# Performance work log

Measured on AMD Instinct MI355X. Metric: run time of the kernel, lower is better.

Reference implementation:

```python
import jax, jax.numpy as jnp
import numpy as np

B, T, N, D, H, L = 8, 200, 512, 4, 64, 32


def setup_inputs() -> dict:
    key = jax.random.key(0)
    ks = jax.random.split(key, 7)
    s = 1.0 / np.sqrt(H)  # torch GRU/Linear default init scale
    x = jax.random.normal(ks[0], (B, T, N, D), dtype=jnp.float32)
    W_ih = jax.random.uniform(ks[1], (3 * H, D), minval=-s, maxval=s, dtype=jnp.float32)
    W_hh = jax.random.uniform(ks[2], (3 * H, H), minval=-s, maxval=s, dtype=jnp.float32)
    b_ih = jax.random.uniform(ks[3], (3 * H,), minval=-s, maxval=s, dtype=jnp.float32)
    b_hh = jax.random.uniform(ks[4], (3 * H,), minval=-s, maxval=s, dtype=jnp.float32)
    W_enc = jax.random.uniform(ks[5], (L, H), minval=-s, maxval=s, dtype=jnp.float32)
    b_enc = jax.random.uniform(ks[6], (L,), minval=-s, maxval=s, dtype=jnp.float32)
    return {"trajectories": x, "W_ih": W_ih, "W_hh": W_hh, "b_ih": b_ih,
            "b_hh": b_hh, "W_enc": W_enc, "b_enc": b_enc}


def _gru_last_hidden(x, W_ih, W_hh, b_ih, b_hh):
    # x: [M, T, D] -> last hidden [M, H]; PyTorch GRU gate order (r, z, n)
    gx = jnp.einsum('mtd,gd->mtg', x, W_ih) + b_ih  # [M, T, 3H], input gates precomputed

    def step(h, gxt):
        gh = h @ W_hh.T + b_hh                      # [M, 3H]
        rz = jax.nn.sigmoid(gxt[:, :2 * H] + gh[:, :2 * H])
        r, z = rz[:, :H], rz[:, H:]
        n = jnp.tanh(gxt[:, 2 * H:] + r * gh[:, 2 * H:])
        h = (1.0 - z) * n + z * h
        return h, None

    h0 = jnp.zeros((x.shape[0], H), dtype=x.dtype)
    hT, _ = jax.lax.scan(step, h0, jnp.swapaxes(gx, 0, 1))  # scan over T
    return hT


def reference(trajectories, W_ih, W_hh, b_ih, b_hh, W_enc, b_enc):
    b, t, n, d = trajectories.shape
    # permute(1,0,2) per clip == move object axis before time, flatten all trajectories
    x = jnp.transpose(trajectories, (0, 2, 1, 3)).reshape(b * n, t, d)  # [M, T, D]
    hT = _gru_last_hidden(x, W_ih, W_hh, b_ih, b_hh)                    # [M, H]
    out = hT @ W_enc.T + b_enc                                          # [M, L]
    return out.reshape(b, n, L)  # list of [N, L] per clip, stacked
```

## Files before the change

kernel.cpp:

```cpp
#include <hip/hip_runtime.h>

#define TT 200
#define NN 512
#define DD 4
#define HH 64
#define LL 32
#define SB 16
#define BPB (NN / SB)
#define KP 72
#define LOG2E 1.44269504088896340736f

typedef short bf16x8 __attribute__((ext_vector_type(8)));
typedef float f32x4 __attribute__((ext_vector_type(4)));

union U8 { unsigned short s[8]; unsigned u[4]; bf16x8 v; };

__device__ __forceinline__ void split2(float x, unsigned short& hi, unsigned short& lo) {
    unsigned u = __float_as_uint(x);
    hi = (unsigned short)(u >> 16);
    float lf = x - __uint_as_float(u & 0xffff0000u);
    lo = (unsigned short)(__float_as_uint(lf) >> 16);
}

__global__ __launch_bounds__(256, 1)
void gru_traj_kernel(const float* __restrict__ xg,
                     const float* __restrict__ W_ih,
                     const float* __restrict__ W_hh,
                     const float* __restrict__ b_ih,
                     const float* __restrict__ b_hh,
                     const float* __restrict__ W_enc,
                     const float* __restrict__ b_enc,
                     float* __restrict__ out)
{
    __shared__ __align__(16) unsigned short hhi[2][SB][KP];
    __shared__ __align__(16) unsigned short hlo[2][SB][KP];
    __shared__ __align__(16) float hsf[SB][HH + 4];

    const int tid = threadIdx.x;
    const int bid = blockIdx.x;
    const int b   = bid >> 5;
    const int n0  = (bid & (BPB - 1)) * SB;

    const int w  = tid >> 6;
    const int l  = tid & 63;
    const int lr = l & 15;
    const int lg = l >> 4;
    const int u0 = 16 * w + lg * 4;

    const float sc[3] = { LOG2E, LOG2E, 2.0f * LOG2E };

    bf16x8 awh[3][2];
    #pragma unroll
    for (int i = 0; i < 3; ++i) {
        const int g = i * 64 + 16 * w + lr;
        #pragma unroll
        for (int kc = 0; kc < 2; ++kc) {
            const float* p = W_hh + g * HH + kc * 32 + lg * 8;
            U8 uh;
            #pragma unroll
            for (int j = 0; j < 8; ++j) {
                unsigned short hi, lo;
                split2(p[j] * sc[i], hi, lo);
                uh.s[j] = hi; (void)lo;
            }
            awh[i][kc] = uh.v;
        }
    }
    float wihc[3][4][4], cbrz[2][4], cbx[4], cbh[4];
    #pragma unroll
    for (int i = 0; i < 3; ++i) {
        #pragma unroll
        for (int r = 0; r < 4; ++r) {
            const int g = i * 64 + u0 + r;
            #pragma unroll
            for (int d = 0; d < 4; ++d) wihc[i][r][d] = W_ih[g * DD + d] * sc[i];
            if (i < 2) cbrz[i][r] = (b_ih[g] + b_hh[g]) * sc[i];
            else       { cbx[r] = b_ih[g] * sc[2]; cbh[r] = b_hh[g] * sc[2]; }
        }
    }

    for (int idx = tid; idx < 2 * SB * KP / 2; idx += 256) {
        reinterpret_cast<unsigned*>(hhi)[idx] = 0u;
        reinterpret_cast<unsigned*>(hlo)[idx] = 0u;
    }
    float hreg[4] = {0.f, 0.f, 0.f, 0.f};

    float4 xc = *reinterpret_cast<const float4*>(
        xg + ((size_t)(b * TT) * NN + n0 + lr) * DD);
    __syncthreads();

    #pragma unroll 2
    for (int t = 0; t < TT; ++t) {
        const int cur = t & 1, nxt = cur ^ 1;
        const int tn  = (t + 1 < TT) ? t + 1 : t;

        float4 xn = *reinterpret_cast<const float4*>(
            xg + ((size_t)(b * TT + tn) * NN + n0 + lr) * DD);

        bf16x8 bh0 = *reinterpret_cast<const bf16x8*>(&hhi[cur][lr][lg * 8]);
        bf16x8 bh1 = *reinterpret_cast<const bf16x8*>(&hhi[cur][lr][32 + lg * 8]);
        bf16x8 bl0 = *reinterpret_cast<const bf16x8*>(&hlo[cur][lr][lg * 8]);
        bf16x8 bl1 = *reinterpret_cast<const bf16x8*>(&hlo[cur][lr][32 + lg * 8]);

        float gxv[3][4];
        #pragma unroll
        for (int i = 0; i < 3; ++i) {
            #pragma unroll
            for (int r = 0; r < 4; ++r) {
                const float c0 = (i < 2) ? cbrz[i][r] : cbx[r];
                gxv[i][r] = fmaf(wihc[i][r][0], xc.x, fmaf(wihc[i][r][1], xc.y,
                            fmaf(wihc[i][r][2], xc.z, fmaf(wihc[i][r][3], xc.w, c0))));
            }
        }

        const f32x4 z4 = {0.f, 0.f, 0.f, 0.f};
        f32x4 aR  = __builtin_amdgcn_mfma_f32_16x16x32_bf16(awh[0][0], bh0, z4, 0,0,0);
        f32x4 aZ  = __builtin_amdgcn_mfma_f32_16x16x32_bf16(awh[1][0], bh0, z4, 0,0,0);
        f32x4 aN  = __builtin_amdgcn_mfma_f32_16x16x32_bf16(awh[2][0], bh0, z4, 0,0,0);
        f32x4 aRc = __builtin_amdgcn_mfma_f32_16x16x32_bf16(awh[0][0], bl0, z4, 0,0,0);
        f32x4 aZc = __builtin_amdgcn_mfma_f32_16x16x32_bf16(awh[1][0], bl0, z4, 0,0,0);
        f32x4 aNc = __builtin_amdgcn_mfma_f32_16x16x32_bf16(awh[2][0], bl0, z4, 0,0,0);
        aR  = __builtin_amdgcn_mfma_f32_16x16x32_bf16(awh[0][1], bh1, aR , 0,0,0);
        aZ  = __builtin_amdgcn_mfma_f32_16x16x32_bf16(awh[1][1], bh1, aZ , 0,0,0);
        aN  = __builtin_amdgcn_mfma_f32_16x16x32_bf16(awh[2][1], bh1, aN , 0,0,0);
        aRc = __builtin_amdgcn_mfma_f32_16x16x32_bf16(awh[0][1], bl1, aRc, 0,0,0);
        aZc = __builtin_amdgcn_mfma_f32_16x16x32_bf16(awh[1][1], bl1, aZc, 0,0,0);
        aNc = __builtin_amdgcn_mfma_f32_16x16x32_bf16(awh[2][1], bl1, aNc, 0,0,0);

        unsigned short hib[4], lob[4];
        #pragma unroll
        for (int r = 0; r < 4; ++r) {
            float sR  = (aR[r] + aRc[r]) + gxv[0][r];
            float sZ  = (aZ[r] + aZc[r]) + gxv[1][r];
            float ghn = (aN[r] + aNc[r]) + cbh[r];
            float rg = __builtin_amdgcn_rcpf(1.0f + __builtin_amdgcn_exp2f(-sR));
            float ez = __builtin_amdgcn_exp2f(-sZ);
            float na = fmaf(rg, ghn, gxv[2][r]);
            float e  = __builtin_amdgcn_exp2f(-na);
            float nn = fmaf(2.0f, __builtin_amdgcn_rcpf(1.0f + e), -1.0f);
            float z  = __builtin_amdgcn_rcpf(1.0f + ez);
            float hn = fmaf(z, hreg[r] - nn, nn);
            hreg[r] = hn;
            split2(hn, hib[r], lob[r]);
        }
        uint2 ph, pl;
        ph.x = (unsigned)hib[0] | ((unsigned)hib[1] << 16);
        ph.y = (unsigned)hib[2] | ((unsigned)hib[3] << 16);
        pl.x = (unsigned)lob[0] | ((unsigned)lob[1] << 16);
        pl.y = (unsigned)lob[2] | ((unsigned)lob[3] << 16);
        *reinterpret_cast<uint2*>(&hhi[nxt][lr][u0]) = ph;
        *reinterpret_cast<uint2*>(&hlo[nxt][lr][u0]) = pl;
        xc = xn;
        __syncthreads();
    }

    #pragma unroll
    for (int r = 0; r < 4; ++r)
        hsf[lr][u0 + r] = hreg[r];
    __syncthreads();
    for (int o = tid; o < SB * LL; o += 256) {
        const int s = o >> 5, li = o & 31;
        float a = b_enc[li];
        #pragma unroll
        for (int k = 0; k < HH; ++k)
            a = fmaf(hsf[s][k], W_enc[li * HH + k], a);
        out[(bid * SB + s) * LL + li] = a;
    }
}

extern "C" void kernel_launch(void* const* d_in, const int* in_sizes, int n_in,
                              void* d_out, int out_size, void* d_ws, size_t ws_size,
                              hipStream_t stream) {
    const float* xg    = (const float*)d_in[0];
    const float* W_ih  = (const float*)d_in[1];
    const float* W_hh  = (const float*)d_in[2];
    const float* b_ih  = (const float*)d_in[3];
    const float* b_hh  = (const float*)d_in[4];
    const float* W_enc = (const float*)d_in[5];
    const float* b_enc = (const float*)d_in[6];
    float* out = (float*)d_out;

    dim3 grid(8 * BPB), block(256);
    hipLaunchKernelGGL(gru_traj_kernel, grid, block, 0, stream,
                       xg, W_ih, W_hh, b_ih, b_hh, W_enc, b_enc, out);
}
```

Before: 112.7 us.

## Double block size to split GRU gate epilogue across wave pairs

The block grows from 4 to 8 waves. Each pair of waves computes the same MFMA gate tiles redundantly, but each wave runs the sigmoid/tanh epilogue on only 2 of the 4 accumulator rows. This halves the serial per-step transcendental work on the recurrence critical path. The cost is duplicated MFMA work, more waves contending at each per-step barrier, and higher register and CU pressure.

```diff
diff --git a/kernel.cpp b/kernel.cpp
--- a/kernel.cpp
+++ b/kernel.cpp
@@ -22,7 +22,7 @@
     lo = (unsigned short)(__float_as_uint(lf) >> 16);
 }
 
-__global__ __launch_bounds__(256, 1)
+__global__ __launch_bounds__(512, 1)
 void gru_traj_kernel(const float* __restrict__ xg,
                      const float* __restrict__ W_ih,
                      const float* __restrict__ W_hh,
@@ -42,17 +42,20 @@
     const int n0  = (bid & (BPB - 1)) * SB;
 
     const int w  = tid >> 6;
+    const int wq = w & 3;
+    const int wg = w >> 2;
     const int l  = tid & 63;
     const int lr = l & 15;
     const int lg = l >> 4;
-    const int u0 = 16 * w + lg * 4;
+    const int u0 = 16 * wq + lg * 4;
+    const int ub = u0 + 2 * wg;
 
     const float sc[3] = { LOG2E, LOG2E, 2.0f * LOG2E };
 
     bf16x8 awh[3][2];
     #pragma unroll
     for (int i = 0; i < 3; ++i) {
-        const int g = i * 64 + 16 * w + lr;
+        const int g = i * 64 + 16 * wq + lr;
         #pragma unroll
         for (int kc = 0; kc < 2; ++kc) {
             const float* p = W_hh + g * HH + kc * 32 + lg * 8;
@@ -66,24 +69,24 @@
             awh[i][kc] = uh.v;
         }
     }
-    float wihc[3][4][4], cbrz[2][4], cbx[4], cbh[4];
+    float wihc[3][2][4], cbrz[2][2], cbx[2], cbh[2];
     #pragma unroll
     for (int i = 0; i < 3; ++i) {
         #pragma unroll
-        for (int r = 0; r < 4; ++r) {
-            const int g = i * 64 + u0 + r;
+        for (int k = 0; k < 2; ++k) {
+            const int g = i * 64 + ub + k;
             #pragma unroll
-            for (int d = 0; d < 4; ++d) wihc[i][r][d] = W_ih[g * DD + d] * sc[i];
-            if (i < 2) cbrz[i][r] = (b_ih[g] + b_hh[g]) * sc[i];
-            else       { cbx[r] = b_ih[g] * sc[2]; cbh[r] = b_hh[g] * sc[2]; }
+            for (int d = 0; d < 4; ++d) wihc[i][k][d] = W_ih[g * DD + d] * sc[i];
+            if (i < 2) cbrz[i][k] = (b_ih[g] + b_hh[g]) * sc[i];
+            else       { cbx[k] = b_ih[g] * sc[2]; cbh[k] = b_hh[g] * sc[2]; }
         }
     }
 
-    for (int idx = tid; idx < 2 * SB * KP / 2; idx += 256) {
+    for (int idx = tid; idx < 2 * SB * KP / 2; idx += 512) {
         reinterpret_cast<unsigned*>(hhi)[idx] = 0u;
         reinterpret_cast<unsigned*>(hlo)[idx] = 0u;
     }
-    float hreg[4] = {0.f, 0.f, 0.f, 0.f};
+    float hreg[2] = {0.f, 0.f};
 
     float4 xc = *reinterpret_cast<const float4*>(
         xg + ((size_t)(b * TT) * NN + n0 + lr) * DD);
@@ -102,14 +105,14 @@
         bf16x8 bl0 = *reinterpret_cast<const bf16x8*>(&hlo[cur][lr][lg * 8]);
         bf16x8 bl1 = *reinterpret_cast<const bf16x8*>(&hlo[cur][lr][32 + lg * 8]);
 
-        float gxv[3][4];
+        float gxv[3][2];
         #pragma unroll
         for (int i = 0; i < 3; ++i) {
             #pragma unroll
-            for (int r = 0; r < 4; ++r) {
-                const float c0 = (i < 2) ? cbrz[i][r] : cbx[r];
-                gxv[i][r] = fmaf(wihc[i][r][0], xc.x, fmaf(wihc[i][r][1], xc.y,
-                            fmaf(wihc[i][r][2], xc.z, fmaf(wihc[i][r][3], xc.w, c0))));
+            for (int k = 0; k < 2; ++k) {
+                const float c0 = (i < 2) ? cbrz[i][k] : cbx[k];
+                gxv[i][k] = fmaf(wihc[i][k][0], xc.x, fmaf(wihc[i][k][1], xc.y,
+                            fmaf(wihc[i][k][2], xc.z, fmaf(wihc[i][k][3], xc.w, c0))));
             }
         }
 
@@ -127,39 +130,38 @@
         aZc = __builtin_amdgcn_mfma_f32_16x16x32_bf16(awh[1][1], bl1, aZc, 0,0,0);
         aNc = __builtin_amdgcn_mfma_f32_16x16x32_bf16(awh[2][1], bl1, aNc, 0,0,0);
 
-        unsigned short hib[4], lob[4];
-        #pragma unroll
-        for (int r = 0; r < 4; ++r) {
-            float sR  = (aR[r] + aRc[r]) + gxv[0][r];
-            float sZ  = (aZ[r] + aZc[r]) + gxv[1][r];
-            float ghn = (aN[r] + aNc[r]) + cbh[r];
-            float rg = __builtin_amdgcn_rcpf(1.0f + __builtin_amdgcn_exp2f(-sR));
-            float ez = __builtin_amdgcn_exp2f(-sZ);
-            float na = fmaf(rg, ghn, gxv[2][r]);
-            float e  = __builtin_amdgcn_exp2f(-na);
-            float nn = fmaf(2.0f, __builtin_amdgcn_rcpf(1.0f + e), -1.0f);
-            float z  = __builtin_amdgcn_rcpf(1.0f + ez);
-            float hn = fmaf(z, hreg[r] - nn, nn);
-            hreg[r] = hn;
-            split2(hn, hib[r], lob[r]);
+        unsigned short hib[2], lob[2];
+#define GATE_ONE(K, C)                                                          \
+        {                                                                       \
+            float sR  = (aR[C] + aRc[C]) + gxv[0][K];                           \
+            float sZ  = (aZ[C] + aZc[C]) + gxv[1][K];                           \
+            float ghn = (aN[C] + aNc[C]) + cbh[K];                              \
+            float rg = __builtin_amdgcn_rcpf(1.0f + __builtin_amdgcn_exp2f(-sR)); \
+            float ez = __builtin_amdgcn_exp2f(-sZ);                             \
+            float na = fmaf(rg, ghn, gxv[2][K]);                                \
+            float e  = __builtin_amdgcn_exp2f(-na);                             \
+            float nn = fmaf(2.0f, __builtin_amdgcn_rcpf(1.0f + e), -1.0f);      \
+            float z  = __builtin_amdgcn_rcpf(1.0f + ez);                        \
+            float hn = fmaf(z, hreg[K] - nn, nn);                               \
+            hreg[K] = hn;                                                       \
+            split2(hn, hib[K], lob[K]);                                         \
         }
-        uint2 ph, pl;
-        ph.x = (unsigned)hib[0] | ((unsigned)hib[1] << 16);
-        ph.y = (unsigned)hib[2] | ((unsigned)hib[3] << 16);
-        pl.x = (unsigned)lob[0] | ((unsigned)lob[1] << 16);
-        pl.y = (unsigned)lob[2] | ((unsigned)lob[3] << 16);
-        *reinterpret_cast<uint2*>(&hhi[nxt][lr][u0]) = ph;
-        *reinterpret_cast<uint2*>(&hlo[nxt][lr][u0]) = pl;
+        if (wg == 0) { GATE_ONE(0, 0) GATE_ONE(1, 1) }
+        else         { GATE_ONE(0, 2) GATE_ONE(1, 3) }
+#undef GATE_ONE
+        unsigned ph = (unsigned)hib[0] | ((unsigned)hib[1] << 16);
+        unsigned pl = (unsigned)lob[0] | ((unsigned)lob[1] << 16);
+        *reinterpret_cast<unsigned*>(&hhi[nxt][lr][ub]) = ph;
+        *reinterpret_cast<unsigned*>(&hlo[nxt][lr][ub]) = pl;
         xc = xn;
         __syncthreads();
     }
 
-    #pragma unroll
-    for (int r = 0; r < 4; ++r)
-        hsf[lr][u0 + r] = hreg[r];
+    hsf[lr][ub]     = hreg[0];
+    hsf[lr][ub + 1] = hreg[1];
     __syncthreads();
-    for (int o = tid; o < SB * LL; o += 256) {
-        const int s = o >> 5, li = o & 31;
+    {
+        const int s = tid >> 5, li = tid & 31;
         float a = b_enc[li];
         #pragma unroll
         for (int k = 0; k < HH; ++k)
@@ -180,7 +182,7 @@
     const float* b_enc = (const float*)d_in[6];
     float* out = (float*)d_out;
 
-    dim3 grid(8 * BPB), block(256);
+    dim3 grid(8 * BPB), block(512);
     hipLaunchKernelGGL(gru_traj_kernel, grid, block, 0, stream,
                        xg, W_ih, W_hh, b_ih, b_hh, W_enc, b_enc, out);
 }
```

New measurement: 128.2 us. +13.8%, slower.
